# Optimization experiments

Hardware: AMD Instinct MI355X
Metric: run time of the kernel (lower is better)

The kernel has to match this reference:

```python
import jax, jax.numpy as jnp
import numpy as np

M0, M1 = 16, 16          # n_modes
C = 64                   # hidden_channels
B = 16                   # batch
H = W = 128              # spatial resolution
SCALE = C ** (-2)        # matches torch: scale * torch.rand(...)


def setup_inputs() -> dict:
    key = jax.random.key(0)
    kx, k0r, k0i, k1r, k1i = jax.random.split(key, 5)
    X = jax.random.normal(kx, (B, C, H, W), dtype=jnp.float32)
    wshape = (C, C, M0, M1)
    # torch.rand with cfloat draws U[0,1) for real and imag parts independently
    w0r = SCALE * jax.random.uniform(k0r, wshape, dtype=jnp.float32)
    w0i = SCALE * jax.random.uniform(k0i, wshape, dtype=jnp.float32)
    w1r = SCALE * jax.random.uniform(k1r, wshape, dtype=jnp.float32)
    w1i = SCALE * jax.random.uniform(k1i, wshape, dtype=jnp.float32)
    return {"X": X, "w0r": w0r, "w0i": w0i, "w1r": w1r, "w1i": w1i}


def reference(X, w0r, w0i, w1r, w1i):
    w0 = w0r + 1j * w0i                       # linear0: (C, C, M0, M1) complex
    w1 = w1r + 1j * w1i                       # linear1
    Xf = jnp.fft.rfftn(X, axes=(-2, -1), norm="forward")   # (B, C, H, W//2+1) complex
    # out[b,c] = sum_t weight[c,t] * Xf[b,t] on the two kept-mode corners
    top = jnp.einsum("ctxy,btxy->bcxy", w0, Xf[:, :, :M0, :M1])
    bot = jnp.einsum("ctxy,btxy->bcxy", w1, Xf[:, :, -M0:, :M1])
    Y = jnp.zeros_like(Xf)
    Y = Y.at[:, :, :M0, :M1].set(top)
    Y = Y.at[:, :, -M0:, :M1].set(bot)
    out = jnp.fft.irfftn(Y, axes=(-2, -1), s=(H, W), norm="forward")
    return out.astype(jnp.float32)
```

## Files before the change

### kernel.cpp

```cpp
#include <hip/hip_runtime.h>

#define PI2 6.28318530717958647692f

__global__ __launch_bounds__(256) void k_fwd(const float* __restrict__ X,
                                             float* __restrict__ Xf) {
  __shared__ __attribute__((aligned(16))) float E1t[64 * 32 * 2];
  __shared__ __attribute__((aligned(16))) float A2t[128 * 34 * 2];
  __shared__ __attribute__((aligned(16))) float E2t[64 * 16 * 2];
  const int plane = blockIdx.x;
  const int tid = threadIdx.x;
  const float* Xp = X + (size_t)plane * (128 * 128);

  #pragma unroll
  for (int k = 0; k < 8; ++k) {
    int idx = tid + k * 256;
    int h = idx >> 5, kxi = idx & 31;
    int kx = kxi + ((kxi >> 4) ? 96 : 0);
    float ang = -PI2 * (float)((kx * h) & 127) / 128.f;
    float s_, c_;
    __sincosf(ang, &s_, &c_);
    E1t[idx * 2] = c_; E1t[idx * 2 + 1] = s_;
  }
  #pragma unroll
  for (int k = 0; k < 4; ++k) {
    int idx = tid + k * 256;
    int w = idx >> 4, ky = idx & 15;
    float ang = -PI2 * (float)((ky * w) & 127) / 128.f;
    float s_, c_;
    __sincosf(ang, &s_, &c_);
    E2t[idx * 2] = c_; E2t[idx * 2 + 1] = s_;
  }
  __syncthreads();

  {
    const int w = tid & 127;
    const int kxg = tid >> 7;
    float cr[16], ci[16];
    #pragma unroll
    for (int j = 0; j < 16; ++j) { cr[j] = 0.f; ci[j] = 0.f; }
    float x0 = Xp[w], x1 = Xp[64 * 128 + w];
    for (int h = 0; h < 64; ++h) {
      float nx0 = 0.f, nx1 = 0.f;
      if (h < 63) { nx0 = Xp[(h + 1) * 128 + w]; nx1 = Xp[(h + 65) * 128 + w]; }
      float ue = x0 + x1;
      float uo = x0 - x1;
      const float4* Erow = (const float4*)&E1t[(h * 32 + kxg * 16) * 2];
      #pragma unroll
      for (int j2 = 0; j2 < 8; ++j2) {
        float4 e = Erow[j2];
        cr[2 * j2]     = fmaf(ue, e.x, cr[2 * j2]);
        ci[2 * j2]     = fmaf(ue, e.y, ci[2 * j2]);
        cr[2 * j2 + 1] = fmaf(uo, e.z, cr[2 * j2 + 1]);
        ci[2 * j2 + 1] = fmaf(uo, e.w, ci[2 * j2 + 1]);
      }
      x0 = nx0; x1 = nx1;
    }
    #pragma unroll
    for (int j = 0; j < 16; ++j) {
      int f2i = w * 34 + kxg * 16 + j;
      A2t[f2i * 2] = cr[j]; A2t[f2i * 2 + 1] = ci[j];
    }
  }
  __syncthreads();

  {
    const int kxi = tid >> 3;
    const int t = tid & 7;
    const float s = (t & 1) ? -1.f : 1.f;
    float r0 = 0.f, i0 = 0.f, r1 = 0.f, i1 = 0.f;
    for (int w = 0; w < 64; ++w) {
      const float2 a = *(const float2*)&A2t[(w * 34 + kxi) * 2];
      const float2 b = *(const float2*)&A2t[((w + 64) * 34 + kxi) * 2];
      float ur = fmaf(s, b.x, a.x);
      float ui = fmaf(s, b.y, a.y);
      const float2 e0 = *(const float2*)&E2t[(w * 16 + t) * 2];
      const float2 e1 = *(const float2*)&E2t[(w * 16 + t + 8) * 2];
      r0 = fmaf(ur, e0.x, r0); r0 = fmaf(-ui, e0.y, r0);
      i0 = fmaf(ur, e0.y, i0); i0 = fmaf(ui, e0.x, i0);
      r1 = fmaf(ur, e1.x, r1); r1 = fmaf(-ui, e1.y, r1);
      i1 = fmaf(ur, e1.y, i1); i1 = fmaf(ui, e1.x, i1);
    }
    const float sc = 1.f / 16384.f;
    float* base = Xf + (size_t)plane * 1024 + kxi * 32;
    *(float2*)&base[t * 2]       = make_float2(r0 * sc, i0 * sc);
    *(float2*)&base[(t + 8) * 2] = make_float2(r1 * sc, i1 * sc);
  }
}

__global__ __launch_bounds__(256) void k_mix(const float* __restrict__ Xf,
                                             const float* __restrict__ w0r,
                                             const float* __restrict__ w0i,
                                             const float* __restrict__ w1r,
                                             const float* __restrict__ w1i,
                                             float* __restrict__ Y) {
  __shared__ __attribute__((aligned(16))) float Wl[4 * 64 * 16 * 2];
  const int bid = blockIdx.x;
  const int c2 = bid >> 8;
  const int x  = (bid >> 4) & 15;
  const int cg = bid & 15;
  const int c0 = cg * 4;
  const int kxi = c2 * 16 + x;
  const float* Wr_g = c2 ? w1r : w0r;
  const float* Wi_g = c2 ? w1i : w0i;
  const int tid = threadIdx.x;
  const int b = tid >> 4;
  const int y = tid & 15;

  #pragma unroll
  for (int k = 0; k < 16; ++k) {
    int idx = tid + k * 256;
    int y_ = idx & 15, t_ = (idx >> 4) & 63, c_ = idx >> 10;
    size_t ga = (((size_t)(c0 + c_) * 64 + t_) * 16 + x) * 16 + y_;
    float wr = Wr_g[ga], wi = Wi_g[ga];
    Wl[idx * 2] = wr; Wl[idx * 2 + 1] = wi;
  }
  __syncthreads();

  float aR[4] = {}, aI[4] = {};
  const float* xbase = Xf + ((size_t)b * 64) * 1024 + kxi * 32 + y * 2;
  for (int t4 = 0; t4 < 64; t4 += 4) {
    float2 xv[4];
    #pragma unroll
    for (int q = 0; q < 4; ++q)
      xv[q] = *(const float2*)&xbase[(size_t)(t4 + q) * 1024];
    #pragma unroll
    for (int q = 0; q < 4; ++q) {
      int t = t4 + q;
      #pragma unroll
      for (int cj = 0; cj < 4; ++cj) {
        const float2 wv = *(const float2*)&Wl[((cj * 64 + t) * 16 + y) * 2];
        aR[cj] = fmaf(xv[q].x, wv.x, aR[cj]);
        aR[cj] = fmaf(-xv[q].y, wv.y, aR[cj]);
        aI[cj] = fmaf(xv[q].x, wv.y, aI[cj]);
        aI[cj] = fmaf(xv[q].y, wv.x, aI[cj]);
      }
    }
  }
  #pragma unroll
  for (int cj = 0; cj < 4; ++cj) {
    size_t ya = ((size_t)(b * 64 + c0 + cj)) * 1024 + kxi * 32 + y * 2;
    *(float2*)&Y[ya] = make_float2(aR[cj], aI[cj]);
  }
}

__global__ __launch_bounds__(256) void k_inv(const float* __restrict__ Y,
                                             float* __restrict__ out) {
  __shared__ __attribute__((aligned(16))) float Yl[1024];
  __shared__ __attribute__((aligned(16))) float Ml[128 * 18 * 2];
  const int plane = blockIdx.x;
  const int tid = threadIdx.x;
  {
    *(float4*)&Yl[tid * 4] = *(const float4*)&Y[(size_t)plane * 1024 + tid * 4];
  }
  __syncthreads();

  {
    const int g = tid >> 7;
    const int h = tid & 127;
    float zr[8] = {}, zi[8] = {};
    float uw, uwi;
    __sincosf(PI2 * (float)h / 128.f, &uwi, &uw);
    const float4* Yl4 = (const float4*)Yl;
    float Tr = 1.f, Ti = 0.f;
    #pragma unroll 4
    for (int kxi = 0; kxi < 16; ++kxi) {
      #pragma unroll
      for (int q = 0; q < 4; ++q) {
        float4 p = Yl4[kxi * 8 + g * 4 + q];
        int m = 2 * q;
        zr[m]   = fmaf(p.x, Tr, zr[m]);   zr[m]   = fmaf(-p.y, Ti, zr[m]);
        zi[m]   = fmaf(p.x, Ti, zi[m]);   zi[m]   = fmaf(p.y, Tr, zi[m]);
        zr[m+1] = fmaf(p.z, Tr, zr[m+1]); zr[m+1] = fmaf(-p.w, Ti, zr[m+1]);
        zi[m+1] = fmaf(p.z, Ti, zi[m+1]); zi[m+1] = fmaf(p.w, Tr, zi[m+1]);
      }
      float nr = Tr * uw - Ti * uwi, ni = Tr * uwi + Ti * uw;
      Tr = nr; Ti = ni;
    }
    __sincosf(PI2 * (float)((112 * h) & 127) / 128.f, &Ti, &Tr);
    #pragma unroll 4
    for (int kxi = 16; kxi < 32; ++kxi) {
      #pragma unroll
      for (int q = 0; q < 4; ++q) {
        float4 p = Yl4[kxi * 8 + g * 4 + q];
        int m = 2 * q;
        zr[m]   = fmaf(p.x, Tr, zr[m]);   zr[m]   = fmaf(-p.y, Ti, zr[m]);
        zi[m]   = fmaf(p.x, Ti, zi[m]);   zi[m]   = fmaf(p.y, Tr, zi[m]);
        zr[m+1] = fmaf(p.z, Tr, zr[m+1]); zr[m+1] = fmaf(-p.w, Ti, zr[m+1]);
        zi[m+1] = fmaf(p.z, Ti, zi[m+1]); zi[m+1] = fmaf(p.w, Tr, zi[m+1]);
      }
      float nr = Tr * uw - Ti * uwi, ni = Tr * uwi + Ti * uw;
      Tr = nr; Ti = ni;
    }
    #pragma unroll
    for (int m = 0; m < 8; ++m) {
      int ky = g * 8 + m;
      float f = (ky == 0) ? 1.f : 2.f;
      int f2i = h * 18 + ky;
      Ml[f2i * 2]     =  f * zr[m];
      Ml[f2i * 2 + 1] = -f * zi[m];
    }
  }
  __syncthreads();

  {
    const int hq = tid >> 6;
    const int w = tid & 63;
    float C[16], S[16];
    {
      float cw, sw;
      __sincosf(PI2 * (float)w / 128.f, &sw, &cw);
      C[0] = 1.f; S[0] = 0.f;
      #pragma unroll
      for (int k = 1; k < 16; ++k) {
        C[k] = C[k - 1] * cw - S[k - 1] * sw;
        S[k] = C[k - 1] * sw + S[k - 1] * cw;
      }
    }
    float* op = out + (size_t)plane * (128 * 128);
    const float4* Ml4 = (const float4*)Ml;
    for (int hj = 0; hj < 32; ++hj) {
      int h = hq * 32 + hj;
      float e = 0.f, o = 0.f;
      #pragma unroll
      for (int j2 = 0; j2 < 8; ++j2) {
        float4 m01 = Ml4[h * 9 + j2];
        int k = 2 * j2;
        float t0 = m01.x * C[k] + m01.y * S[k];
        float t1 = m01.z * C[k + 1] + m01.w * S[k + 1];
        e += t0; o += t1;
      }
      op[h * 128 + w]      = e + o;
      op[h * 128 + w + 64] = e - o;
    }
  }
}

extern "C" void kernel_launch(void* const* d_in, const int* in_sizes, int n_in,
                              void* d_out, int out_size, void* d_ws, size_t ws_size,
                              hipStream_t stream) {
  const float* X   = (const float*)d_in[0];
  const float* w0r = (const float*)d_in[1];
  const float* w0i = (const float*)d_in[2];
  const float* w1r = (const float*)d_in[3];
  const float* w1i = (const float*)d_in[4];
  float* outp = (float*)d_out;
  float* Xf = (float*)d_ws;
  float* Yw = (float*)d_ws + (1u << 20);
  k_fwd<<<1024, 256, 0, stream>>>(X, Xf);
  k_mix<<<512, 256, 0, stream>>>(Xf, w0r, w0i, w1r, w1i, Yw);
  k_inv<<<1024, 256, 0, stream>>>(Yw, outp);
}
```

Before: 183.1 us.

## Register-block forward column DFT over two columns and drop E2 twiddle table

In the forward kernel, each thread now handles two adjacent columns with float2 loads against 8 kx frequencies instead of one column against 16. This halves the shared twiddle reads per FMA. The second-stage twiddle table is replaced by an in-register complex rotation recurrence, and the A2t padding changes from 34 to 33, which reduces shared memory. The mix kernel batches 8 Xf loads per iteration instead of 4, and a few divisions become reciprocal multiplies. The recurrence may accumulate slight rounding error over the 64 steps.

Result: no change. 184.3 us (+0.7%).

```diff
diff --git a/kernel.cpp b/kernel.cpp
--- a/kernel.cpp
+++ b/kernel.cpp
@@ -5,8 +5,7 @@
 __global__ __launch_bounds__(256) void k_fwd(const float* __restrict__ X,
                                              float* __restrict__ Xf) {
   __shared__ __attribute__((aligned(16))) float E1t[64 * 32 * 2];
-  __shared__ __attribute__((aligned(16))) float A2t[128 * 34 * 2];
-  __shared__ __attribute__((aligned(16))) float E2t[64 * 16 * 2];
+  __shared__ __attribute__((aligned(16))) float A2t[128 * 33 * 2];
   const int plane = blockIdx.x;
   const int tid = threadIdx.x;
   const float* Xp = X + (size_t)plane * (128 * 128);
@@ -15,50 +14,55 @@
   for (int k = 0; k < 8; ++k) {
     int idx = tid + k * 256;
     int h = idx >> 5, kxi = idx & 31;
-    int kx = kxi + ((kxi >> 4) ? 96 : 0);
-    float ang = -PI2 * (float)((kx * h) & 127) / 128.f;
+    int kx = kxi + ((kxi & 16) ? 96 : 0);
     float s_, c_;
-    __sincosf(ang, &s_, &c_);
+    __sincosf(-PI2 * (float)((kx * h) & 127) * (1.f / 128.f), &s_, &c_);
     E1t[idx * 2] = c_; E1t[idx * 2 + 1] = s_;
   }
-  #pragma unroll
-  for (int k = 0; k < 4; ++k) {
-    int idx = tid + k * 256;
-    int w = idx >> 4, ky = idx & 15;
-    float ang = -PI2 * (float)((ky * w) & 127) / 128.f;
-    float s_, c_;
-    __sincosf(ang, &s_, &c_);
-    E2t[idx * 2] = c_; E2t[idx * 2 + 1] = s_;
-  }
-  __syncthreads();
-
-  {
-    const int w = tid & 127;
-    const int kxg = tid >> 7;
-    float cr[16], ci[16];
-    #pragma unroll
-    for (int j = 0; j < 16; ++j) { cr[j] = 0.f; ci[j] = 0.f; }
-    float x0 = Xp[w], x1 = Xp[64 * 128 + w];
+  __syncthreads();
+
+  {
+    const int w2 = tid & 63;
+    const int kxg = tid >> 6;
+    float cr[8][2], ci[8][2];
+    #pragma unroll
+    for (int j = 0; j < 8; ++j) {
+      cr[j][0] = cr[j][1] = 0.f; ci[j][0] = ci[j][1] = 0.f;
+    }
+    float2 xa = *(const float2*)&Xp[w2 * 2];
+    float2 xb = *(const float2*)&Xp[64 * 128 + w2 * 2];
     for (int h = 0; h < 64; ++h) {
-      float nx0 = 0.f, nx1 = 0.f;
-      if (h < 63) { nx0 = Xp[(h + 1) * 128 + w]; nx1 = Xp[(h + 65) * 128 + w]; }
-      float ue = x0 + x1;
-      float uo = x0 - x1;
-      const float4* Erow = (const float4*)&E1t[(h * 32 + kxg * 16) * 2];
-      #pragma unroll
-      for (int j2 = 0; j2 < 8; ++j2) {
-        float4 e = Erow[j2];
-        cr[2 * j2]     = fmaf(ue, e.x, cr[2 * j2]);
-        ci[2 * j2]     = fmaf(ue, e.y, ci[2 * j2]);
-        cr[2 * j2 + 1] = fmaf(uo, e.z, cr[2 * j2 + 1]);
-        ci[2 * j2 + 1] = fmaf(uo, e.w, ci[2 * j2 + 1]);
-      }
-      x0 = nx0; x1 = nx1;
-    }
-    #pragma unroll
-    for (int j = 0; j < 16; ++j) {
-      int f2i = w * 34 + kxg * 16 + j;
-      A2t[f2i * 2] = cr[j]; A2t[f2i * 2 + 1] = ci[j];
+      float2 na = make_float2(0.f, 0.f), nb = make_float2(0.f, 0.f);
+      if (h < 63) {
+        na = *(const float2*)&Xp[(h + 1) * 128 + w2 * 2];
+        nb = *(const float2*)&Xp[(h + 65) * 128 + w2 * 2];
+      }
+      float ue0 = xa.x + xb.x, ue1 = xa.y + xb.y;
+      float uo0 = xa.x - xb.x, uo1 = xa.y - xb.y;
+      const float4* Er = (const float4*)&E1t[(h * 32 + kxg * 8) * 2];
+      #pragma unroll
+      for (int j2 = 0; j2 < 4; ++j2) {
+        float4 e = Er[j2];
+        int je = 2 * j2, jo = 2 * j2 + 1;
+        cr[je][0] = fmaf(ue0, e.x, cr[je][0]);
+        ci[je][0] = fmaf(ue0, e.y, ci[je][0]);
+        cr[je][1] = fmaf(ue1, e.x, cr[je][1]);
+        ci[je][1] = fmaf(ue1, e.y, ci[je][1]);
+        cr[jo][0] = fmaf(uo0, e.z, cr[jo][0]);
+        ci[jo][0] = fmaf(uo0, e.w, ci[jo][0]);
+        cr[jo][1] = fmaf(uo1, e.z, cr[jo][1]);
+        ci[jo][1] = fmaf(uo1, e.w, ci[jo][1]);
+      }
+      xa = na; xb = nb;
+    }
+    #pragma unroll
+    for (int u = 0; u < 2; ++u) {
+      int w = 2 * w2 + u;
+      #pragma unroll
+      for (int j = 0; j < 8; ++j) {
+        int f2i = w * 33 + 8 * kxg + j;
+        A2t[f2i * 2] = cr[j][u]; A2t[f2i * 2 + 1] = ci[j][u];
+      }
     }
   }
   __syncthreads();
@@ -67,18 +71,24 @@
     const int kxi = tid >> 3;
     const int t = tid & 7;
     const float s = (t & 1) ? -1.f : 1.f;
+    float d0r, d0i, d1r, d1i;
+    __sincosf(-PI2 * (float)t * (1.f / 128.f), &d0i, &d0r);
+    __sincosf(-PI2 * (float)(t + 8) * (1.f / 128.f), &d1i, &d1r);
+    float T0r = 1.f, T0i = 0.f, T1r = 1.f, T1i = 0.f;
     float r0 = 0.f, i0 = 0.f, r1 = 0.f, i1 = 0.f;
+    #pragma unroll 4
     for (int w = 0; w < 64; ++w) {
-      const float2 a = *(const float2*)&A2t[(w * 34 + kxi) * 2];
-      const float2 b = *(const float2*)&A2t[((w + 64) * 34 + kxi) * 2];
+      const float2 a = *(const float2*)&A2t[(w * 33 + kxi) * 2];
+      const float2 b = *(const float2*)&A2t[((w + 64) * 33 + kxi) * 2];
       float ur = fmaf(s, b.x, a.x);
       float ui = fmaf(s, b.y, a.y);
-      const float2 e0 = *(const float2*)&E2t[(w * 16 + t) * 2];
-      const float2 e1 = *(const float2*)&E2t[(w * 16 + t + 8) * 2];
-      r0 = fmaf(ur, e0.x, r0); r0 = fmaf(-ui, e0.y, r0);
-      i0 = fmaf(ur, e0.y, i0); i0 = fmaf(ui, e0.x, i0);
-      r1 = fmaf(ur, e1.x, r1); r1 = fmaf(-ui, e1.y, r1);
-      i1 = fmaf(ur, e1.y, i1); i1 = fmaf(ui, e1.x, i1);
+      r0 = fmaf(ur, T0r, r0); r0 = fmaf(-ui, T0i, r0);
+      i0 = fmaf(ur, T0i, i0); i0 = fmaf(ui, T0r, i0);
+      r1 = fmaf(ur, T1r, r1); r1 = fmaf(-ui, T1i, r1);
+      i1 = fmaf(ur, T1i, i1); i1 = fmaf(ui, T1r, i1);
+      float n0r = T0r * d0r - T0i * d0i, n0i = T0r * d0i + T0i * d0r;
+      float n1r = T1r * d1r - T1i * d1i, n1i = T1r * d1i + T1i * d1r;
+      T0r = n0r; T0i = n0i; T1r = n1r; T1i = n1i;
     }
     const float sc = 1.f / 16384.f;
     float* base = Xf + (size_t)plane * 1024 + kxi * 32;
@@ -118,14 +128,14 @@
 
   float aR[4] = {}, aI[4] = {};
   const float* xbase = Xf + ((size_t)b * 64) * 1024 + kxi * 32 + y * 2;
-  for (int t4 = 0; t4 < 64; t4 += 4) {
-    float2 xv[4];
-    #pragma unroll
-    for (int q = 0; q < 4; ++q)
-      xv[q] = *(const float2*)&xbase[(size_t)(t4 + q) * 1024];
-    #pragma unroll
-    for (int q = 0; q < 4; ++q) {
-      int t = t4 + q;
+  for (int t8 = 0; t8 < 64; t8 += 8) {
+    float2 xv[8];
+    #pragma unroll
+    for (int q = 0; q < 8; ++q)
+      xv[q] = *(const float2*)&xbase[(size_t)(t8 + q) * 1024];
+    #pragma unroll
+    for (int q = 0; q < 8; ++q) {
+      int t = t8 + q;
       #pragma unroll
       for (int cj = 0; cj < 4; ++cj) {
         const float2 wv = *(const float2*)&Wl[((cj * 64 + t) * 16 + y) * 2];
@@ -159,7 +169,7 @@
     const int h = tid & 127;
     float zr[8] = {}, zi[8] = {};
     float uw, uwi;
-    __sincosf(PI2 * (float)h / 128.f, &uwi, &uw);
+    __sincosf(PI2 * (float)h * (1.f / 128.f), &uwi, &uw);
     const float4* Yl4 = (const float4*)Yl;
     float Tr = 1.f, Ti = 0.f;
     #pragma unroll 4
@@ -176,7 +186,7 @@
       float nr = Tr * uw - Ti * uwi, ni = Tr * uwi + Ti * uw;
       Tr = nr; Ti = ni;
     }
-    __sincosf(PI2 * (float)((112 * h) & 127) / 128.f, &Ti, &Tr);
+    __sincosf(PI2 * (float)((112 * h) & 127) * (1.f / 128.f), &Ti, &Tr);
     #pragma unroll 4
     for (int kxi = 16; kxi < 32; ++kxi) {
       #pragma unroll
@@ -208,7 +218,7 @@
     float C[16], S[16];
     {
       float cw, sw;
-      __sincosf(PI2 * (float)w / 128.f, &sw, &cw);
+      __sincosf(PI2 * (float)w * (1.f / 128.f), &sw, &cw);
       C[0] = 1.f; S[0] = 0.f;
       #pragma unroll
       for (int k = 1; k < 16; ++k) {
@@ -218,6 +228,7 @@
     }
     float* op = out + (size_t)plane * (128 * 128);
     const float4* Ml4 = (const float4*)Ml;
+    #pragma unroll 2
     for (int hj = 0; hj < 32; ++hj) {
       int h = hq * 32 + hj;
       float e = 0.f, o = 0.f;
```
